# Kernel tuning notes

Measured on AMD Instinct MI355X. Metric: run time of the kernel, lower is better.

## Reference

```python
import jax, jax.numpy as jnp
import numpy as np
import math

D = 1280      # embed_dim ('650M')
H = 20        # n_head
DH = D // H   # d_hidden = 64
DFF = 4 * D   # r_ff = 4
LN_EPS = 1e-5


def layer_norm(x, gamma, beta):
    mu = jnp.mean(x, axis=-1, keepdims=True)
    var = jnp.var(x, axis=-1, keepdims=True)
    return (x - mu) * jax.lax.rsqrt(var + LN_EPS) * gamma + beta


def setup_inputs() -> dict:
    key = jax.random.key(0)
    ks = jax.random.split(key, 16)
    B, L = 2, 2048
    x = jax.random.normal(ks[0], (B, L, D), dtype=jnp.float32)
    y = jax.random.normal(ks[1], (B, L, D), dtype=jnp.float32)  # dm_embeds (unused by module)
    s_qkv = 1.0 / math.sqrt(D)
    Wq = jax.random.uniform(ks[2], (D, D), jnp.float32, -s_qkv, s_qkv)
    Wk = jax.random.uniform(ks[3], (D, D), jnp.float32, -s_qkv, s_qkv)
    Wv = jax.random.uniform(ks[4], (D, D), jnp.float32, -s_qkv, s_qkv)
    Wo = jax.random.uniform(ks[5], (D, D), jnp.float32, -s_qkv, s_qkv)
    bo = jnp.zeros((D,), jnp.float32)
    W1 = jax.random.normal(ks[6], (D, DFF), jnp.float32) * math.sqrt(2.0 / D)  # kaiming
    b1 = jnp.zeros((DFF,), jnp.float32)
    W2 = jax.random.uniform(ks[7], (DFF, D), jnp.float32, -1.0 / math.sqrt(DFF), 1.0 / math.sqrt(DFF))
    b2 = jnp.zeros((D,), jnp.float32)
    g1 = jnp.ones((D,), jnp.float32); be1 = jnp.zeros((D,), jnp.float32)
    g2 = jnp.ones((D,), jnp.float32); be2 = jnp.zeros((D,), jnp.float32)
    return dict(x=x, y=y, Wq=Wq, Wk=Wk, Wv=Wv, Wo=Wo, bo=bo,
                W1=W1, b1=b1, W2=W2, b2=b2, g1=g1, be1=be1, g2=g2, be2=be2)


def reference(x, y, Wq, Wk, Wv, Wo, bo, W1, b1, W2, b2, g1, be1, g2, be2):
    B, L, _ = x.shape
    scaling = 1.0 / math.sqrt(DH)
    # --- pre-norm self-attention ---
    xn = layer_norm(x, g1, be1)
    q = (xn @ Wq).reshape(B, L, H, DH) * scaling
    k = (xn @ Wk).reshape(B, L, H, DH)
    v = (xn @ Wv).reshape(B, L, H, DH)
    scores = jnp.einsum('bqhd,bkhd->bhqk', q, k)
    attn = jax.nn.softmax(scores, axis=-1)
    o = jnp.einsum('bhqk,bkhd->bqhd', attn, v).reshape(B, L, D)
    x = x + (o @ Wo + bo)
    # --- pre-norm FFN ---
    xn = layer_norm(x, g2, be2)
    h = jax.nn.relu(xn @ W1 + b1)
    x = x + (h @ W2 + b2)
    return x
```

## Files before the change

### kernel.cpp

```cpp
#include <hip/hip_runtime.h>

typedef short bf16x8 __attribute__((ext_vector_type(8)));
typedef short bf16x4 __attribute__((ext_vector_type(4)));
typedef float f32x4 __attribute__((ext_vector_type(4)));
typedef unsigned short u16;

#define GL16(g, l) __builtin_amdgcn_global_load_lds( \
    (const __attribute__((address_space(1))) void*)(g), \
    (__attribute__((address_space(3))) void*)(l), 16, 0, 0)

__device__ __forceinline__ u16 f2bf(float f) {
  union { float f; unsigned u; } v; v.f = f;
  return (u16)((v.u + 0x7fffu + ((v.u >> 16) & 1u)) >> 16);
}

__device__ __forceinline__ float exp2_(float x) {
#if __has_builtin(__builtin_amdgcn_exp2f)
  return __builtin_amdgcn_exp2f(x);
#else
  return __expf(x * 0.69314718056f);
#endif
}

__device__ __forceinline__ unsigned cvtpk(float a, float b) {
  unsigned r;
  asm("v_cvt_pk_bf16_f32 %0, %1, %2" : "=v"(r) : "v"(a), "v"(b));
  return r;
}

__global__ __launch_bounds__(256) void ln_kernel(
    const float* __restrict__ x, const float* __restrict__ g,
    const float* __restrict__ b, u16* __restrict__ out) {
  const int row = blockIdx.x, tid = threadIdx.x;
  const float4* xr = (const float4*)(x + (size_t)row * 1280);
  float4 v1 = xr[tid];
  float4 v2 = make_float4(0.f, 0.f, 0.f, 0.f);
  if (tid < 64) v2 = xr[256 + tid];
  float s = v1.x + v1.y + v1.z + v1.w + v2.x + v2.y + v2.z + v2.w;
  float q = v1.x * v1.x + v1.y * v1.y + v1.z * v1.z + v1.w * v1.w +
            v2.x * v2.x + v2.y * v2.y + v2.z * v2.z + v2.w * v2.w;
#pragma unroll
  for (int off = 32; off >= 1; off >>= 1) {
    s += __shfl_xor(s, off);
    q += __shfl_xor(q, off);
  }
  __shared__ float sm[8];
  if ((tid & 63) == 0) { sm[tid >> 6] = s; sm[4 + (tid >> 6)] = q; }
  __syncthreads();
  s = sm[0] + sm[1] + sm[2] + sm[3];
  q = sm[4] + sm[5] + sm[6] + sm[7];
  const float mean = s * (1.0f / 1280.0f);
  const float rstd = rsqrtf(q * (1.0f / 1280.0f) - mean * mean + 1e-5f);
  const float4* gr = (const float4*)g;
  const float4* br = (const float4*)b;
  u16* orow = out + (size_t)row * 1280;
  {
    float4 gg = gr[tid], bb = br[tid];
    ushort4 o;
    o.x = f2bf((v1.x - mean) * rstd * gg.x + bb.x);
    o.y = f2bf((v1.y - mean) * rstd * gg.y + bb.y);
    o.z = f2bf((v1.z - mean) * rstd * gg.z + bb.z);
    o.w = f2bf((v1.w - mean) * rstd * gg.w + bb.w);
    *(ushort4*)&orow[tid * 4] = o;
  }
  if (tid < 64) {
    float4 gg = gr[256 + tid], bb = br[256 + tid];
    ushort4 o;
    o.x = f2bf((v2.x - mean) * rstd * gg.x + bb.x);
    o.y = f2bf((v2.y - mean) * rstd * gg.y + bb.y);
    o.z = f2bf((v2.z - mean) * rstd * gg.z + bb.z);
    o.w = f2bf((v2.w - mean) * rstd * gg.w + bb.w);
    *(ushort4*)&orow[(256 + tid) * 4] = o;
  }
}

__global__ __launch_bounds__(256) void tconv_kernel(
    const float* __restrict__ src, u16* __restrict__ dst,
    int rows, int cols, float scale) {
  __shared__ float t[64][33];
  const int tid = threadIdx.x;
  const size_t c0 = (size_t)blockIdx.x * 64, r0 = (size_t)blockIdx.y * 32;
  const int ty = tid >> 4, col4 = tid & 15;
#pragma unroll
  for (int i = 0; i < 2; ++i) {
    const int row = ty + i * 16;
    float4 v = *(const float4*)&src[(r0 + row) * cols + c0 + col4 * 4];
    t[col4 * 4 + 0][row] = v.x;
    t[col4 * 4 + 1][row] = v.y;
    t[col4 * 4 + 2][row] = v.z;
    t[col4 * 4 + 3][row] = v.w;
  }
  __syncthreads();
  const int c = tid >> 2, rb = (tid & 3) * 8;
  ushort4 o1, o2;
  o1.x = f2bf(t[c][rb + 0] * scale); o1.y = f2bf(t[c][rb + 1] * scale);
  o1.z = f2bf(t[c][rb + 2] * scale); o1.w = f2bf(t[c][rb + 3] * scale);
  o2.x = f2bf(t[c][rb + 4] * scale); o2.y = f2bf(t[c][rb + 5] * scale);
  o2.z = f2bf(t[c][rb + 6] * scale); o2.w = f2bf(t[c][rb + 7] * scale);
  u16* d = &dst[(c0 + c) * rows + r0 + rb];
  *(ushort4*)d = o1;
  *(ushort4*)(d + 4) = o2;
}

__global__ __launch_bounds__(256) void vtrans_kernel(const u16* __restrict__ qkv,
                                                     u16* __restrict__ vt) {
  __shared__ u16 t[64][65];
  const int tx = threadIdx.x & 63, ty = threadIdx.x >> 6;
  const int t0 = blockIdx.x * 64, bh = blockIdx.y, b = bh / 20, h = bh % 20;
  const u16* src = qkv + (size_t)b * 2048 * 3840 + 2560 + h * 64;
  for (int i = ty; i < 64; i += 4) t[i][tx] = src[(size_t)(t0 + i) * 3840 + tx];
  __syncthreads();
  u16* dst = vt + (size_t)bh * 64 * 2048 + t0;
  for (int i = ty; i < 64; i += 4) dst[(size_t)i * 2048 + tx] = t[tx][i];
}

__global__ __launch_bounds__(256) void initadd_kernel(
    const float* __restrict__ src, const float* __restrict__ bias,
    float* __restrict__ out) {
  const size_t i = (size_t)blockIdx.x * 256 + threadIdx.x;
  float4 v = ((const float4*)src)[i];
  float4 b = ((const float4*)bias)[i % 320];
  v.x += b.x; v.y += b.y; v.z += b.z; v.w += b.w;
  ((float4*)out)[i] = v;
}

template <int EPI>
__device__ __forceinline__ void gemm_body(
    const u16* __restrict__ A, const u16* __restrict__ BT,
    const float* __restrict__ bias, void* __restrict__ out,
    int M, int N, int K, int kSteps) {
  __shared__ __attribute__((aligned(16))) u16 Als[3][128 * 32];
  __shared__ __attribute__((aligned(16))) u16 Bls[3][128 * 32];
  const int tid = threadIdx.x;
  const int w = tid >> 6, lane = tid & 63;
  const int lo = lane & 15, hi = lane >> 4;
  const int wm = w >> 1, wn = w & 1;
  const int gx = gridDim.x, gxy = gx * gridDim.y;
  const int nwg = gxy * gridDim.z;
  int s = blockIdx.x + gx * blockIdx.y + gxy * blockIdx.z;
  s = (s & 7) * (nwg >> 3) + (s >> 3);
  const int bz = s / gxy; s -= bz * gxy;
  const int by = s / gx;  const int bx = s - by * gx;
  const size_t m0 = (size_t)by * 128, n0 = (size_t)bx * 128;
  const int kt0 = bz * kSteps;
  f32x4 acc[4][4] = {};
  const int srow = w * 32 + (lane >> 2);
  const int scol = ((lane & 3) ^ ((lane >> 3) & 3)) * 8;
  const int rsw = (lo >> 1) & 3;
#define STAGE(buf, kt)                                                        \
  do {                                                                        \
    const size_t kb = (size_t)(kt) * 32 + scol;                               \
    GL16(&A[(m0 + srow) * K + kb],       &Als[buf][(w * 2 + 0) * 512]);       \
    GL16(&A[(m0 + srow + 16) * K + kb],  &Als[buf][(w * 2 + 1) * 512]);       \
    GL16(&BT[(n0 + srow) * K + kb],      &Bls[buf][(w * 2 + 0) * 512]);       \
    GL16(&BT[(n0 + srow + 16) * K + kb], &Bls[buf][(w * 2 + 1) * 512]);       \
  } while (0)
  STAGE(0, kt0 + 0);
  STAGE(1, kt0 + 1);
  int cur = 0;
  for (int t = 0; t < kSteps; ++t) {
    if (t + 1 < kSteps) asm volatile("s_waitcnt vmcnt(4)" ::: "memory");
    else                asm volatile("s_waitcnt vmcnt(0)" ::: "memory");
    __builtin_amdgcn_s_barrier();
    __builtin_amdgcn_sched_barrier(0);
    const int nxt = (cur == 0) ? 2 : cur - 1;
    if (t + 2 < kSteps) STAGE(nxt, kt0 + t + 2);
    bf16x8 af[4], bfr[4];
#pragma unroll
    for (int mi = 0; mi < 4; ++mi)
      af[mi] = *(const bf16x8*)&Als[cur][(wm * 64 + mi * 16 + lo) * 32 + ((hi ^ rsw) * 8)];
#pragma unroll
    for (int ni = 0; ni < 4; ++ni)
      bfr[ni] = *(const bf16x8*)&Bls[cur][(wn * 64 + ni * 16 + lo) * 32 + ((hi ^ rsw) * 8)];
#pragma unroll
    for (int mi = 0; mi < 4; ++mi)
#pragma unroll
      for (int ni = 0; ni < 4; ++ni)
        acc[mi][ni] = __builtin_amdgcn_mfma_f32_16x16x32_bf16(
            af[mi], bfr[ni], acc[mi][ni], 0, 0, 0);
    cur = (cur == 2) ? 0 : cur + 1;
  }
#undef STAGE
#pragma unroll
  for (int ni = 0; ni < 4; ++ni) {
    const size_t col = n0 + wn * 64 + ni * 16 + lo;
    const float bv = (EPI == 1) ? bias[col] : 0.0f;
#pragma unroll
    for (int mi = 0; mi < 4; ++mi) {
      const size_t rb = m0 + wm * 64 + mi * 16 + hi * 4;
#pragma unroll
      for (int r = 0; r < 4; ++r) {
        const size_t idx = (rb + r) * N + col;
        float v = acc[mi][ni][r];
        if (EPI == 0) {
          ((u16*)out)[idx] = f2bf(v);
        } else if (EPI == 1) {
          v += bv;
          v = fmaxf(v, 0.0f);
          ((u16*)out)[idx] = f2bf(v);
        } else {
          atomicAdd(&((float*)out)[idx], v);
        }
      }
    }
  }
}

__global__ __launch_bounds__(256, 3) void gemm_qkv(
    const u16* __restrict__ A, const u16* __restrict__ BT,
    void* __restrict__ out, int M, int N, int K, int kSteps) {
  gemm_body<0>(A, BT, nullptr, out, M, N, K, kSteps);
}
__global__ __launch_bounds__(256, 3) void gemm_oproj(
    const u16* __restrict__ A, const u16* __restrict__ BT,
    void* __restrict__ out, int M, int N, int K, int kSteps) {
  gemm_body<3>(A, BT, nullptr, out, M, N, K, kSteps);
}
__global__ __launch_bounds__(256, 3) void gemm_ffn1(
    const u16* __restrict__ A, const u16* __restrict__ BT,
    const float* __restrict__ bias, void* __restrict__ out,
    int M, int N, int K, int kSteps) {
  gemm_body<1>(A, BT, bias, out, M, N, K, kSteps);
}
__global__ __launch_bounds__(256, 3) void gemm_ffn2(
    const u16* __restrict__ A, const u16* __restrict__ BT,
    void* __restrict__ out, int M, int N, int K, int kSteps) {
  gemm_body<3>(A, BT, nullptr, out, M, N, K, kSteps);
}

__global__ __launch_bounds__(256) void attn_kernel(
    const u16* __restrict__ qkv, const u16* __restrict__ vt,
    u16* __restrict__ aout) {
  __shared__ __attribute__((aligned(16))) u16 Klds[64 * 64];
  __shared__ __attribute__((aligned(16))) u16 Vlds[64 * 64];
  __shared__ __attribute__((aligned(16))) u16 Plds[4][16][72];
  const int tid = threadIdx.x;
  const int w = tid >> 6, lane = tid & 63;
  const int lo = lane & 15, hi = lane >> 4;
  const int bh = blockIdx.x, qt = blockIdx.y;
  const int b = bh / 20, h = bh % 20;
  const size_t qrow = (size_t)b * 2048 + qt * 64 + w * 16 + lo;
  bf16x8 qf[2];
  qf[0] = *(const bf16x8*)&qkv[qrow * 3840 + h * 64 + hi * 8];
  qf[1] = *(const bf16x8*)&qkv[qrow * 3840 + h * 64 + 32 + hi * 8];
  float m_i = -1e30f, l_i = 0.0f;
  f32x4 accO[4] = {};
  const int srow = lane >> 3;
  const int scol = ((lane & 7) ^ srow) * 8;
  const u16* kbase = qkv + (size_t)b * 2048 * 3840 + 1280 + h * 64;
  const u16* vbase = vt + (size_t)bh * 64 * 2048;
  for (int kt = 0; kt < 32; ++kt) {
#pragma unroll
    for (int c = 0; c < 2; ++c) {
      const int chunk = w * 2 + c;
      const int row = chunk * 8 + srow;
      GL16(kbase + (size_t)(kt * 64 + row) * 3840 + scol, &Klds[chunk * 512]);
      GL16(vbase + (size_t)row * 2048 + kt * 64 + scol, &Vlds[chunk * 512]);
    }
    __syncthreads();
    f32x4 s4[4] = {};
#pragma unroll
    for (int st = 0; st < 4; ++st) {
      const int row = st * 16 + lo;
      const int sw = (row & 7) << 3;
#pragma unroll
      for (int ks = 0; ks < 2; ++ks) {
        bf16x8 a = *(const bf16x8*)&Klds[row * 64 + ((ks * 32 + hi * 8) ^ sw)];
        s4[st] = __builtin_amdgcn_mfma_f32_16x16x32_bf16(a, qf[ks], s4[st], 0, 0, 0);
      }
    }
    float tm = fmaxf(fmaxf(fmaxf(s4[0][0], s4[0][1]), fmaxf(s4[0][2], s4[0][3])),
                     fmaxf(fmaxf(s4[1][0], s4[1][1]), fmaxf(s4[1][2], s4[1][3])));
    tm = fmaxf(tm, fmaxf(fmaxf(fmaxf(s4[2][0], s4[2][1]), fmaxf(s4[2][2], s4[2][3])),
                         fmaxf(fmaxf(s4[3][0], s4[3][1]), fmaxf(s4[3][2], s4[3][3]))));
    tm = fmaxf(tm, __shfl_xor(tm, 16));
    tm = fmaxf(tm, __shfl_xor(tm, 32));
    if (!__all(tm <= m_i + 8.0f)) {
      const float mnew = fmaxf(m_i, tm);
      const float corr = exp2_(m_i - mnew);
      m_i = mnew;
      l_i *= corr;
      float cr[4];
#pragma unroll
      for (int r = 0; r < 4; ++r) cr[r] = __shfl(corr, hi * 4 + r);
#pragma unroll
      for (int d = 0; d < 4; ++d)
#pragma unroll
        for (int r = 0; r < 4; ++r) accO[d][r] *= cr[r];
    }
#pragma unroll
    for (int st = 0; st < 4; ++st)
#pragma unroll
      for (int r = 0; r < 4; ++r) {
        const float p = exp2_(s4[st][r] - m_i);
        s4[st][r] = p;
        l_i += p;
      }
#pragma unroll
    for (int st = 0; st < 4; ++st) {
      uint2 pk;
      pk.x = cvtpk(s4[st][0], s4[st][1]);
      pk.y = cvtpk(s4[st][2], s4[st][3]);
      *(uint2*)&Plds[w][lo][st * 16 + hi * 4] = pk;
    }
    asm volatile("s_waitcnt lgkmcnt(0)" ::: "memory");
    __builtin_amdgcn_sched_barrier(0);
#pragma unroll
    for (int ks = 0; ks < 2; ++ks) {
      bf16x8 pa = *(const bf16x8*)&Plds[w][lo][ks * 32 + hi * 8];
#pragma unroll
      for (int d = 0; d < 4; ++d) {
        const int row = d * 16 + lo;
        bf16x8 vb = *(const bf16x8*)
            &Vlds[row * 64 + ((ks * 32 + hi * 8) ^ ((row & 7) << 3))];
        accO[d] = __builtin_amdgcn_mfma_f32_16x16x32_bf16(pa, vb, accO[d], 0, 0, 0);
      }
    }
    __syncthreads();
  }
  l_i += __shfl_xor(l_i, 16);
  l_i += __shfl_xor(l_i, 32);
  float linv[4];
#pragma unroll
  for (int r = 0; r < 4; ++r) linv[r] = 1.0f / __shfl(l_i, hi * 4 + r);
  const size_t orow0 = (size_t)b * 2048 + qt * 64 + w * 16 + hi * 4;
#pragma unroll
  for (int d = 0; d < 4; ++d)
#pragma unroll
    for (int r = 0; r < 4; ++r)
      aout[(orow0 + r) * 1280 + h * 64 + d * 16 + lo] =
          f2bf(accO[d][r] * linv[r]);
}

extern "C" void kernel_launch(void* const* d_in, const int* in_sizes, int n_in,
                              void* d_out, int out_size, void* d_ws, size_t ws_size,
                              hipStream_t stream) {
  const float* x   = (const float*)d_in[0];
  const float* Wq  = (const float*)d_in[2];
  const float* Wk  = (const float*)d_in[3];
  const float* Wv  = (const float*)d_in[4];
  const float* Wo  = (const float*)d_in[5];
  const float* bo  = (const float*)d_in[6];
  const float* W1  = (const float*)d_in[7];
  const float* b1  = (const float*)d_in[8];
  const float* W2  = (const float*)d_in[9];
  const float* b2  = (const float*)d_in[10];
  const float* g1  = (const float*)d_in[11];
  const float* be1 = (const float*)d_in[12];
  const float* g2  = (const float*)d_in[13];
  const float* be2 = (const float*)d_in[14];

  u16* xn   = (u16*)d_ws;
  u16* Wqkv = xn + (size_t)4096 * 1280;
  u16* WoT  = Wqkv + (size_t)3840 * 1280;
  u16* W1T  = WoT + (size_t)1280 * 1280;
  u16* W2T  = W1T + (size_t)5120 * 1280;
  u16* aOut = W2T + (size_t)1280 * 5120;
  float* x1 = (float*)(aOut + (size_t)4096 * 1280);
  u16* qkvb = (u16*)(x1 + (size_t)4096 * 1280);
  u16* vtb  = qkvb + (size_t)4096 * 3840;
  u16* hbuf = qkvb;

  const float qscale = 0.125f * 1.4426950408889634f;
  ln_kernel<<<4096, 256, 0, stream>>>(x, g1, be1, xn);
  tconv_kernel<<<dim3(20, 40), 256, 0, stream>>>(Wq, Wqkv, 1280, 1280, qscale);
  tconv_kernel<<<dim3(20, 40), 256, 0, stream>>>(Wk, Wqkv + (size_t)1280 * 1280, 1280, 1280, 1.0f);
  tconv_kernel<<<dim3(20, 40), 256, 0, stream>>>(Wv, Wqkv + (size_t)2 * 1280 * 1280, 1280, 1280, 1.0f);
  tconv_kernel<<<dim3(20, 40), 256, 0, stream>>>(Wo, WoT, 1280, 1280, 1.0f);
  tconv_kernel<<<dim3(80, 40), 256, 0, stream>>>(W1, W1T, 1280, 5120, 1.0f);
  tconv_kernel<<<dim3(20, 160), 256, 0, stream>>>(W2, W2T, 5120, 1280, 1.0f);
  gemm_qkv<<<dim3(30, 32, 1), 256, 0, stream>>>(xn, Wqkv, qkvb, 4096, 3840, 1280, 40);
  vtrans_kernel<<<dim3(32, 40), 256, 0, stream>>>(qkvb, vtb);
  attn_kernel<<<dim3(40, 32), 256, 0, stream>>>(qkvb, vtb, aOut);
  initadd_kernel<<<5120, 256, 0, stream>>>(x, bo, x1);
  gemm_oproj<<<dim3(10, 32, 2), 256, 0, stream>>>(aOut, WoT, x1, 4096, 1280, 1280, 20);
  ln_kernel<<<4096, 256, 0, stream>>>(x1, g2, be2, xn);
  gemm_ffn1<<<dim3(40, 32, 1), 256, 0, stream>>>(xn, W1T, b1, hbuf, 4096, 5120, 1280, 40);
  initadd_kernel<<<5120, 256, 0, stream>>>(x1, b2, (float*)d_out);
  gemm_ffn2<<<dim3(10, 32, 2), 256, 0, stream>>>(hbuf, W2T, d_out, 4096, 1280, 5120, 80);
  (void)in_sizes; (void)n_in; (void)out_size; (void)ws_size;
}
```

Before: 415.6 us.

## Use 256x128 tile GEMM with triple-buffered LDS for QKV and FFN1

Adds a larger-tile GEMM body (256x128 output per workgroup, 8x4 MFMA fragments per wave) with a three-stage LDS pipeline and an XCD-aware block swizzle, used for the QKV and FFN1 projections. The bigger tile raises arithmetic intensity and cuts global/LDS traffic per FLOP. The deeper prefetch is meant to hide load latency. In exchange it uses more registers and LDS, lowering occupancy to 2 blocks per CU, and halves the grid size, which may leave CUs underfilled.

```diff
diff --git a/kernel.cpp b/kernel.cpp
--- a/kernel.cpp
+++ b/kernel.cpp
@@ -206,21 +206,103 @@
   }
 }
 
-__global__ __launch_bounds__(256, 3) void gemm_qkv(
+template <int EPI>
+__device__ __forceinline__ void gemm_big_body(
+    const u16* __restrict__ A, const u16* __restrict__ BT,
+    const float* __restrict__ bias, void* __restrict__ out,
+    int M, int N, int K, int kSteps) {
+  __shared__ __attribute__((aligned(16))) u16 Als[3][256 * 32];
+  __shared__ __attribute__((aligned(16))) u16 Bls[3][128 * 32];
+  const int tid = threadIdx.x;
+  const int w = tid >> 6, lane = tid & 63;
+  const int lo = lane & 15, hi = lane >> 4;
+  const int wm = w >> 1, wn = w & 1;
+  const int gx = gridDim.x;
+  const int nwg = gx * gridDim.y;
+  int s = blockIdx.x + gx * blockIdx.y;
+  s = (s & 7) * (nwg >> 3) + (s >> 3);
+  const int by = s / gx;  const int bx = s - by * gx;
+  const size_t m0 = (size_t)by * 256, n0 = (size_t)bx * 128;
+  f32x4 acc[8][4] = {};
+  const int crow = lane >> 2;
+  const int scol = ((lane & 3) ^ ((lane >> 3) & 3)) * 8;
+  const int rsw = (lo >> 1) & 3;
+#define STAGEB(buf, kt)                                                       \
+  do {                                                                        \
+    const size_t kb = (size_t)(kt) * 32 + scol;                               \
+    _Pragma("unroll")                                                         \
+    for (int i = 0; i < 4; ++i)                                               \
+      GL16(&A[(m0 + w * 64 + i * 16 + crow) * K + kb],                        \
+           &Als[buf][(w * 4 + i) * 512]);                                     \
+    _Pragma("unroll")                                                         \
+    for (int i = 0; i < 2; ++i)                                               \
+      GL16(&BT[(n0 + w * 32 + i * 16 + crow) * K + kb],                       \
+           &Bls[buf][(w * 2 + i) * 512]);                                     \
+  } while (0)
+  STAGEB(0, 0);
+  STAGEB(1, 1);
+  int cur = 0;
+  for (int t = 0; t < kSteps; ++t) {
+    if (t + 1 < kSteps) asm volatile("s_waitcnt vmcnt(6)" ::: "memory");
+    else                asm volatile("s_waitcnt vmcnt(0)" ::: "memory");
+    __builtin_amdgcn_s_barrier();
+    __builtin_amdgcn_sched_barrier(0);
+    const int nxt = (cur == 0) ? 2 : cur - 1;
+    if (t + 2 < kSteps) STAGEB(nxt, t + 2);
+    bf16x8 af[8], bfr[4];
+#pragma unroll
+    for (int mi = 0; mi < 8; ++mi)
+      af[mi] = *(const bf16x8*)&Als[cur][(wm * 128 + mi * 16 + lo) * 32 + ((hi ^ rsw) * 8)];
+#pragma unroll
+    for (int ni = 0; ni < 4; ++ni)
+      bfr[ni] = *(const bf16x8*)&Bls[cur][(wn * 64 + ni * 16 + lo) * 32 + ((hi ^ rsw) * 8)];
+#pragma unroll
+    for (int mi = 0; mi < 8; ++mi)
+#pragma unroll
+      for (int ni = 0; ni < 4; ++ni)
+        acc[mi][ni] = __builtin_amdgcn_mfma_f32_16x16x32_bf16(
+            af[mi], bfr[ni], acc[mi][ni], 0, 0, 0);
+    cur = (cur == 2) ? 0 : cur + 1;
+  }
+#undef STAGEB
+#pragma unroll
+  for (int ni = 0; ni < 4; ++ni) {
+    const size_t col = n0 + wn * 64 + ni * 16 + lo;
+    const float bv = (EPI == 1) ? bias[col] : 0.0f;
+#pragma unroll
+    for (int mi = 0; mi < 8; ++mi) {
+      const size_t rb = m0 + wm * 128 + mi * 16 + hi * 4;
+#pragma unroll
+      for (int r = 0; r < 4; ++r) {
+        const size_t idx = (rb + r) * N + col;
+        float v = acc[mi][ni][r];
+        if (EPI == 0) {
+          ((u16*)out)[idx] = f2bf(v);
+        } else if (EPI == 1) {
+          v += bv;
+          v = fmaxf(v, 0.0f);
+          ((u16*)out)[idx] = f2bf(v);
+        }
+      }
+    }
+  }
+}
+
+__global__ __launch_bounds__(256, 2) void gemm_qkv(
     const u16* __restrict__ A, const u16* __restrict__ BT,
     void* __restrict__ out, int M, int N, int K, int kSteps) {
-  gemm_body<0>(A, BT, nullptr, out, M, N, K, kSteps);
+  gemm_big_body<0>(A, BT, nullptr, out, M, N, K, kSteps);
+}
+__global__ __launch_bounds__(256, 2) void gemm_ffn1(
+    const u16* __restrict__ A, const u16* __restrict__ BT,
+    const float* __restrict__ bias, void* __restrict__ out,
+    int M, int N, int K, int kSteps) {
+  gemm_big_body<1>(A, BT, bias, out, M, N, K, kSteps);
 }
 __global__ __launch_bounds__(256, 3) void gemm_oproj(
     const u16* __restrict__ A, const u16* __restrict__ BT,
     void* __restrict__ out, int M, int N, int K, int kSteps) {
   gemm_body<3>(A, BT, nullptr, out, M, N, K, kSteps);
-}
-__global__ __launch_bounds__(256, 3) void gemm_ffn1(
-    const u16* __restrict__ A, const u16* __restrict__ BT,
-    const float* __restrict__ bias, void* __restrict__ out,
-    int M, int N, int K, int kSteps) {
-  gemm_body<1>(A, BT, bias, out, M, N, K, kSteps);
 }
 __global__ __launch_bounds__(256, 3) void gemm_ffn2(
     const u16* __restrict__ A, const u16* __restrict__ BT,
@@ -369,13 +451,13 @@
   tconv_kernel<<<dim3(20, 40), 256, 0, stream>>>(Wo, WoT, 1280, 1280, 1.0f);
   tconv_kernel<<<dim3(80, 40), 256, 0, stream>>>(W1, W1T, 1280, 5120, 1.0f);
   tconv_kernel<<<dim3(20, 160), 256, 0, stream>>>(W2, W2T, 5120, 1280, 1.0f);
-  gemm_qkv<<<dim3(30, 32, 1), 256, 0, stream>>>(xn, Wqkv, qkvb, 4096, 3840, 1280, 40);
+  gemm_qkv<<<dim3(30, 16), 256, 0, stream>>>(xn, Wqkv, qkvb, 4096, 3840, 1280, 40);
   vtrans_kernel<<<dim3(32, 40), 256, 0, stream>>>(qkvb, vtb);
   attn_kernel<<<dim3(40, 32), 256, 0, stream>>>(qkvb, vtb, aOut);
   initadd_kernel<<<5120, 256, 0, stream>>>(x, bo, x1);
   gemm_oproj<<<dim3(10, 32, 2), 256, 0, stream>>>(aOut, WoT, x1, 4096, 1280, 1280, 20);
   ln_kernel<<<4096, 256, 0, stream>>>(x1, g2, be2, xn);
-  gemm_ffn1<<<dim3(40, 32, 1), 256, 0, stream>>>(xn, W1T, b1, hbuf, 4096, 5120, 1280, 40);
+  gemm_ffn1<<<dim3(40, 16), 256, 0, stream>>>(xn, W1T, b1, hbuf, 4096, 5120, 1280, 40);
   initadd_kernel<<<5120, 256, 0, stream>>>(x1, b2, (float*)d_out);
   gemm_ffn2<<<dim3(10, 32, 2), 256, 0, stream>>>(hbuf, W2T, d_out, 4096, 1280, 5120, 80);
   (void)in_sizes; (void)n_in; (void)out_size; (void)ws_size;
```

New measurement: 414.2 us. Within noise of the previous version (-0.3%).
